# Optimization experiments

Hardware: AMD Instinct MI355X
Metric: run time of the kernel (lower is better)

The kernel has to match this reference:

```python
import jax, jax.numpy as jnp
import numpy as np

N_NODES = 50000


def _gcn_layer(x, W, b, src, dst, n_nodes):
    # GCNConv: h = D^{-1/2} (A + I) D^{-1/2} (x W) + b, with src/dst already
    # including self-loops.
    h = x @ W  # [N, out]
    deg = jax.ops.segment_sum(jnp.ones(src.shape, x.dtype), dst,
                              num_segments=n_nodes)  # [N]
    dinv = jnp.where(deg > 0, jax.lax.rsqrt(jnp.maximum(deg, 1e-12)), 0.0)
    norm = dinv[src] * dinv[dst]  # [E+N]
    msg = h[src] * norm[:, None]  # gathered + weighted messages
    out = jax.ops.segment_sum(msg, dst, num_segments=n_nodes)  # scatter-add
    return out + b


def setup_inputs() -> dict:
    key = jax.random.key(0)
    k0, k1, k2, k3 = jax.random.split(key, 4)
    d_in, hidden, n_edges = 128, 128, 800000
    x = jax.random.normal(k0, (N_NODES, d_in), dtype=jnp.float32)
    edge_index = jax.random.randint(k1, (2, n_edges), 0, N_NODES, dtype=jnp.int64)
    W1 = jax.random.normal(k2, (d_in, hidden), dtype=jnp.float32) * (1.0 / np.sqrt(d_in))
    b1 = jnp.zeros((hidden,), jnp.float32)
    W2 = jax.random.normal(k3, (hidden, hidden), dtype=jnp.float32) * (1.0 / np.sqrt(hidden))
    b2 = jnp.zeros((hidden,), jnp.float32)
    return {"x": x, "edge_index": edge_index, "W1": W1, "b1": b1,
            "W2": W2, "b2": b2}


def reference(x, edge_index, W1, b1, W2, b2):
    n = x.shape[0]
    loop = jnp.arange(n, dtype=edge_index.dtype)
    src = jnp.concatenate([edge_index[0], loop])  # add self-loops
    dst = jnp.concatenate([edge_index[1], loop])
    h = _gcn_layer(x, W1, b1, src, dst, n)
    h = jax.nn.relu(h)
    # dropout p=0.5 is identity in eval mode (self.training == False)
    h = _gcn_layer(h, W2, b2, src, dst, n)
    return jax.nn.log_softmax(h, axis=1)
```

## Files before the change

### kernel.cpp

```cpp
#include <hip/hip_runtime.h>
#include <math.h>

#define D 128
#define CAP 6144
#define EPB 4096

typedef __attribute__((ext_vector_type(8))) short bf16x8;
typedef __attribute__((ext_vector_type(4))) float f32x4;

__device__ __forceinline__ float bf_lo(unsigned u) { return __uint_as_float(u << 16); }
__device__ __forceinline__ float bf_hi(unsigned u) { return __uint_as_float(u & 0xFFFF0000u); }
__device__ __forceinline__ unsigned pack_bf16(float a, float b) {
    unsigned ua = __float_as_uint(a), ub = __float_as_uint(b);
    ua = (ua + 0x7FFFu + ((ua >> 16) & 1u)) >> 16;
    ub = (ub + 0x7FFFu + ((ub >> 16) & 1u)) >> 16;
    return ua | (ub << 16);
}

__device__ __forceinline__ int edge_at(const void* eidx, int i64, long long pos) {
    return i64 ? (int)((const long long*)eidx)[pos] : ((const int*)eidx)[pos];
}


__global__ void k_init(const int* e32, int* flag, int* bcnt) {
    int t = threadIdx.x;
    bcnt[t] = 0;
    if (t == 0) {
        int f = 1;
        #pragma unroll
        for (int j = 1; j < 32; j += 2)
            if (e32[j] != 0) f = 0;
        *flag = f;
    }
}


template <int AF32>
__device__ __forceinline__ void gemm_body(char* lds, int bid, const void* Ain,
                                          const float* __restrict__ Wf,
                                          unsigned* __restrict__ yout, int n) {
    int tid = threadIdx.x;
    #pragma unroll
    for (int it = 0; it < 32; ++it) {
        int idx = tid + it * 256;
        int c = idx & 127, k2 = idx >> 7;
        *(unsigned*)&lds[c * 272 + k2 * 4] =
            pack_bf16(Wf[(k2 * 2) * D + c], Wf[(k2 * 2 + 1) * D + c]);
    }
    int w = tid >> 6, l = tid & 63;
    int row0 = bid * 128;
    int rowA0 = row0 + w * 16 + (l & 15);
    int rowA1 = rowA0 + 64;
    int rA0 = rowA0 < n ? rowA0 : 0;
    int rA1 = rowA1 < n ? rowA1 : 0;
    __syncthreads();

    f32x4 acc[2][8];
    #pragma unroll
    for (int r = 0; r < 2; ++r)
        #pragma unroll
        for (int f = 0; f < 8; ++f) acc[r][f] = (f32x4)0.f;

    #pragma unroll
    for (int s = 0; s < 4; ++s) {
        bf16x8 a0, a1;
        if (AF32) {
            const float* Af = (const float*)Ain;
            const float4* p0 = (const float4*)(Af + (size_t)rA0 * D + ((l >> 4) << 3) + s * 32);
            const float4* p1 = (const float4*)(Af + (size_t)rA1 * D + ((l >> 4) << 3) + s * 32);
            float4 f0 = p0[0], f1 = p0[1], f2 = p1[0], f3 = p1[1];
            uint4 v0, v1;
            v0.x = pack_bf16(f0.x, f0.y); v0.y = pack_bf16(f0.z, f0.w);
            v0.z = pack_bf16(f1.x, f1.y); v0.w = pack_bf16(f1.z, f1.w);
            v1.x = pack_bf16(f2.x, f2.y); v1.y = pack_bf16(f2.z, f2.w);
            v1.z = pack_bf16(f3.x, f3.y); v1.w = pack_bf16(f3.z, f3.w);
            a0 = *(bf16x8*)&v0;
            a1 = *(bf16x8*)&v1;
        } else {
            const char* Ab = (const char*)Ain;
            a0 = *(const bf16x8*)(Ab + (size_t)rA0 * 256 + ((l >> 4) << 4) + s * 64);
            a1 = *(const bf16x8*)(Ab + (size_t)rA1 * 256 + ((l >> 4) << 4) + s * 64);
        }
        int boff = ((l >> 4) << 4) + s * 64;
        #pragma unroll
        for (int f = 0; f < 8; ++f) {
            bf16x8 b = *(const bf16x8*)&lds[(f * 16 + (l & 15)) * 272 + boff];
            acc[0][f] = __builtin_amdgcn_mfma_f32_16x16x32_bf16(a0, b, acc[0][f], 0, 0, 0);
            acc[1][f] = __builtin_amdgcn_mfma_f32_16x16x32_bf16(a1, b, acc[1][f], 0, 0, 0);
        }
    }

    float* fl = (float*)lds;
    #pragma unroll
    for (int r = 0; r < 2; ++r) {
        __syncthreads();
        {
            int rbase = w * 16 + ((l >> 4) << 2);
            #pragma unroll
            for (int f = 0; f < 8; ++f) {
                int c = f * 16 + (l & 15);
                #pragma unroll
                for (int j = 0; j < 4; ++j)
                    fl[(rbase + j) * 132 + c] = acc[r][f][j];
            }
        }
        __syncthreads();
        int row = tid >> 2, cseg = (tid & 3) << 5;
        int gr = row0 + r * 64 + row;
        if (gr < n) {
            uint4* ob = (uint4*)yout + (size_t)gr * 16 + ((tid & 3) << 2);
            #pragma unroll
            for (int q = 0; q < 4; ++q) {
                uint4 v;
                v.x = pack_bf16(fl[row * 132 + cseg + q * 8 + 0], fl[row * 132 + cseg + q * 8 + 1]);
                v.y = pack_bf16(fl[row * 132 + cseg + q * 8 + 2], fl[row * 132 + cseg + q * 8 + 3]);
                v.z = pack_bf16(fl[row * 132 + cseg + q * 8 + 4], fl[row * 132 + cseg + q * 8 + 5]);
                v.w = pack_bf16(fl[row * 132 + cseg + q * 8 + 6], fl[row * 132 + cseg + q * 8 + 7]);
                ob[q] = v;
            }
        }
    }
}


__global__ void __launch_bounds__(256) k_prep(const void* eidx, const int* flag,
                                              int* bcnt,
                                              unsigned* __restrict__ binned, int e,
                                              const float* __restrict__ x,
                                              const float* __restrict__ W1,
                                              unsigned* __restrict__ y1,
                                              int n, int ebk) {
    __shared__ char lds[35840];
    int b = blockIdx.x, t = threadIdx.x;

    if (b < ebk) {
        int* hist = (int*)lds;
        int* gbase = hist + 256;
        int* lcur = gbase + 256;
        uint2* ed = (uint2*)(lds + 3072);
        hist[t] = 0;
        lcur[t] = 0;
        __syncthreads();
        long long base = (long long)b * EPB;
        int i64 = *flag;
        #pragma unroll
        for (int k = 0; k < EPB / 256; ++k) {
            long long i = base + k * 256 + t;
            if (i < e) {
                int s = edge_at(eidx, i64, i);
                int d = edge_at(eidx, i64, (long long)e + i);
                ed[k * 256 + t] = make_uint2((unsigned)s, (unsigned)d);
                atomicAdd(&hist[d >> 8], 1);
            }
        }
        __syncthreads();
        int c = hist[t];
        gbase[t] = c ? atomicAdd(&bcnt[t], c) : 0;
        __syncthreads();
        long long rem = e - base;
        int lim = (rem < EPB) ? (int)rem : EPB;
        for (int j = t; j < lim; j += 256) {
            uint2 sd = ed[j];
            int bk = sd.y >> 8;
            int off = gbase[bk] + atomicAdd(&lcur[bk], 1);
            if (off >= CAP) off = CAP - 1;
            binned[(size_t)bk * CAP + off] = sd.x | ((sd.y & 255u) << 17);
        }
    } else {
        gemm_body<1>(lds, b - ebk, x, W1, y1, n);
    }
}


__global__ void __launch_bounds__(256) k_binB(const unsigned* __restrict__ binned,
                                              const int* __restrict__ bcnt,
                                              unsigned* __restrict__ meta,
                                              unsigned* __restrict__ csr64,
                                              int n) {
    __shared__ int lcur[256];
    int b = blockIdx.x, t = threadIdx.x;
    lcur[t] = 0;
    __syncthreads();

    int cnt = bcnt[b];
    if (cnt > CAP) cnt = CAP;
    unsigned nodebase = (unsigned)b << 8;
    for (int i = t; i < cnt; i += 256) {
        unsigned en = binned[(size_t)b * CAP + i];
        unsigned src = en & 0x1FFFF;
        unsigned dl = en >> 17;
        int pos = atomicAdd(&lcur[dl], 1);
        unsigned node = nodebase + dl;
        if (pos < 64)
            csr64[(size_t)node * 64 + pos] = src;
    }
    __syncthreads();

    int node = b * 256 + t;
    if (node < n) {
        int dv = lcur[t];
        unsigned q = __float2uint_rn(rsqrtf((float)(dv + 1)) * 32767.0f);
        meta[node] = (q << 17) | (unsigned)(dv < 64 ? dv : 64);
        int filled = dv < 64 ? dv : 64;
        int pend = (filled + 15) & ~15;
        for (int j = filled; j < pend; ++j)
            csr64[(size_t)node * 64 + j] = (unsigned)node;
    }
}


template <int EPI>
__global__ void __launch_bounds__(256) k_agg(const unsigned* __restrict__ Y,
                                             const unsigned* __restrict__ meta,
                                             const unsigned* __restrict__ csr64,
                                             const float* __restrict__ bias,
                                             void* __restrict__ outp, int n) {
    int node = blockIdx.x * 4 + (threadIdx.x >> 6);
    if (node >= n) return;
    int lane = threadIdx.x & 63;
    int l16 = lane & 15;
    unsigned mt = meta[node];
    unsigned us = Y[(size_t)node * 64 + lane];
    const unsigned* cp = csr64 + (size_t)node * 64;
    unsigned g0 = cp[l16];
    unsigned g1 = cp[16 + l16];

    int cdeg = mt & 0x1FFFF;
    float di = (float)(mt >> 17) * (1.0f / 32767.0f);
    int gcnt = (cdeg + 15) >> 4;
    float ax = 0.f, ay = 0.f;

#define PROCA(gv, base)                                                        \
    {                                                                          \
        unsigned uu[16], qq[16];                                               \
        _Pragma("unroll") for (int k2 = 0; k2 < 16; ++k2) {                    \
            unsigned s_ = __shfl((gv), k2, 16) & 0x1FFFF;                      \
            uu[k2] = Y[(size_t)s_ * 64 + lane];                                \
            qq[k2] = meta[s_];                                                 \
        }                                                                      \
        _Pragma("unroll") for (int k2 = 0; k2 < 16; ++k2) {                    \
            float w_ = ((base) + k2 < cdeg)                                    \
                           ? (float)(qq[k2] >> 17) * (1.0f / 32767.0f) : 0.f;  \
            ax += w_ * bf_lo(uu[k2]);                                          \
            ay += w_ * bf_hi(uu[k2]);                                          \
        }                                                                      \
    }

    if (gcnt > 0) PROCA(g0, 0);
    if (gcnt > 1) PROCA(g1, 16);
    if (gcnt > 2) {
        unsigned g2 = cp[32 + l16];
        if (gcnt > 3) {
            unsigned g3 = cp[48 + l16];
            PROCA(g2, 32);
            PROCA(g3, 48);
        } else {
            PROCA(g2, 32);
        }
    }
#undef PROCA

    float2 bv = ((const float2*)bias)[lane];
    float z0 = (ax + di * bf_lo(us)) * di + bv.x;
    float z1 = (ay + di * bf_hi(us)) * di + bv.y;

    if (EPI == 0) {
        ((unsigned*)outp)[(size_t)node * 64 + lane] =
            pack_bf16(fmaxf(z0, 0.f), fmaxf(z1, 0.f));
    } else {
        float m = fmaxf(z0, z1);
        #pragma unroll
        for (int off = 1; off < 64; off <<= 1) m = fmaxf(m, __shfl_xor(m, off));
        float s = __expf(z0 - m) + __expf(z1 - m);
        #pragma unroll
        for (int off = 1; off < 64; off <<= 1) s += __shfl_xor(s, off);
        float lse = m + __logf(s);
        ((float2*)outp)[(size_t)node * 64 + lane] = make_float2(z0 - lse, z1 - lse);
    }
}


__global__ void __launch_bounds__(256) k_gemm2(const unsigned* __restrict__ h,
                                               const float* __restrict__ W2,
                                               unsigned* __restrict__ y2, int n) {
    __shared__ char lds[34816];
    gemm_body<0>(lds, blockIdx.x, h, W2, y2, n);
}


extern "C" void kernel_launch(void* const* d_in, const int* in_sizes, int n_in,
                              void* d_out, int out_size, void* d_ws, size_t ws_size,
                              hipStream_t stream) {
    const float* x  = (const float*)d_in[0];
    const void* eix = d_in[1];
    const float* W1 = (const float*)d_in[2];
    const float* b1 = (const float*)d_in[3];
    const float* W2 = (const float*)d_in[4];
    const float* b2 = (const float*)d_in[5];
    float* out = (float*)d_out;
    int n = in_sizes[0] / D;
    int e = in_sizes[1] / 2;

    char* p = (char*)d_ws;
    auto carve = [&](size_t bytes) -> void* {
        void* r = (void*)p;
        p += (bytes + 255) & ~(size_t)255;
        return r;
    };
    int*      flag   = (int*)carve(4);
    unsigned* meta   = (unsigned*)carve((size_t)n * 4);
    int*      bcnt   = (int*)carve(1024);
    unsigned* csr64  = (unsigned*)carve((size_t)n * 64 * 4);
    unsigned* binned = (unsigned*)carve((size_t)256 * CAP * 4);
    unsigned* y1     = (unsigned*)carve((size_t)n * 64 * 4);
    unsigned* h      = (unsigned*)carve((size_t)n * 64 * 4);

    int nb = (n + 255) / 256;
    int ebk = (e + EPB - 1) / EPB;
    int gb = (n + 127) / 128;
    int ab = (n + 3) / 4;

    k_init<<<1, 256, 0, stream>>>((const int*)eix, flag, bcnt);
    k_prep<<<ebk + gb, 256, 0, stream>>>(eix, flag, bcnt, binned, e, x, W1, y1, n, ebk);
    k_binB<<<nb, 256, 0, stream>>>(binned, bcnt, meta, csr64, n);
    k_agg<0><<<ab, 256, 0, stream>>>(y1, meta, csr64, b1, h, n);
    k_gemm2<<<gb, 256, 0, stream>>>(h, W2, y1, n);
    k_agg<1><<<ab, 256, 0, stream>>>(y1, meta, csr64, b2, out, n);
}
```

Measured before the change: 135.3 us.

## Move layer-1 GEMM into CSR-build kernel and simplify aggregation to scalar-indexed loop

The layer-1 GEMM blocks now launch together with the CSR build (k_mid) instead of with the edge-binning pass. The edge-binning kernel becomes its own smaller launch. The aggregation kernel makes the node index wave-uniform and reads neighbor indices as scalars in 4-way unrolled loops. This replaces the 16-wide shuffle batches and drops the CSR padding writes. The per-edge scale factor is folded into a single final multiply. The intent is to balance the work that overlaps across the launch stages and to cut wasted padded gathers, at the cost of fewer gathers in flight per iteration.

```diff
diff --git a/kernel.cpp b/kernel.cpp
--- a/kernel.cpp
+++ b/kernel.cpp
@@ -31,6 +31,46 @@
         for (int j = 1; j < 32; j += 2)
             if (e32[j] != 0) f = 0;
         *flag = f;
+    }
+}
+
+
+__global__ void __launch_bounds__(256) k_prep(const void* eidx, const int* flag,
+                                              int* bcnt,
+                                              unsigned* __restrict__ binned, int e) {
+    __shared__ int hist[256];
+    __shared__ int gbase[256];
+    __shared__ int lcur[256];
+    __shared__ uint2 ed[EPB];
+    int b = blockIdx.x, t = threadIdx.x;
+
+    hist[t] = 0;
+    lcur[t] = 0;
+    __syncthreads();
+    long long base = (long long)b * EPB;
+    int i64 = *flag;
+    #pragma unroll
+    for (int k = 0; k < EPB / 256; ++k) {
+        long long i = base + k * 256 + t;
+        if (i < e) {
+            int s = edge_at(eidx, i64, i);
+            int d = edge_at(eidx, i64, (long long)e + i);
+            ed[k * 256 + t] = make_uint2((unsigned)s, (unsigned)d);
+            atomicAdd(&hist[d >> 8], 1);
+        }
+    }
+    __syncthreads();
+    int c = hist[t];
+    gbase[t] = c ? atomicAdd(&bcnt[t], c) : 0;
+    __syncthreads();
+    long long rem = e - base;
+    int lim = (rem < EPB) ? (int)rem : EPB;
+    for (int j = t; j < lim; j += 256) {
+        uint2 sd = ed[j];
+        int bk = sd.y >> 8;
+        int off = gbase[bk] + atomicAdd(&lcur[bk], 1);
+        if (off >= CAP) off = CAP - 1;
+        binned[(size_t)bk * CAP + off] = sd.x | ((sd.y & 255u) << 17);
     }
 }
 
@@ -123,62 +163,21 @@
 }
 
 
-__global__ void __launch_bounds__(256) k_prep(const void* eidx, const int* flag,
-                                              int* bcnt,
-                                              unsigned* __restrict__ binned, int e,
-                                              const float* __restrict__ x,
-                                              const float* __restrict__ W1,
-                                              unsigned* __restrict__ y1,
-                                              int n, int ebk) {
-    __shared__ char lds[35840];
+__global__ void __launch_bounds__(256) k_mid(const unsigned* __restrict__ binned,
+                                             const int* __restrict__ bcnt,
+                                             unsigned* __restrict__ meta,
+                                             unsigned* __restrict__ csr64,
+                                             const float* __restrict__ x,
+                                             const float* __restrict__ W1,
+                                             unsigned* __restrict__ y1,
+                                             int n, int nb) {
+    __shared__ char lds[34816];
     int b = blockIdx.x, t = threadIdx.x;
-
-    if (b < ebk) {
-        int* hist = (int*)lds;
-        int* gbase = hist + 256;
-        int* lcur = gbase + 256;
-        uint2* ed = (uint2*)(lds + 3072);
-        hist[t] = 0;
-        lcur[t] = 0;
-        __syncthreads();
-        long long base = (long long)b * EPB;
-        int i64 = *flag;
-        #pragma unroll
-        for (int k = 0; k < EPB / 256; ++k) {
-            long long i = base + k * 256 + t;
-            if (i < e) {
-                int s = edge_at(eidx, i64, i);
-                int d = edge_at(eidx, i64, (long long)e + i);
-                ed[k * 256 + t] = make_uint2((unsigned)s, (unsigned)d);
-                atomicAdd(&hist[d >> 8], 1);
-            }
-        }
-        __syncthreads();
-        int c = hist[t];
-        gbase[t] = c ? atomicAdd(&bcnt[t], c) : 0;
-        __syncthreads();
-        long long rem = e - base;
-        int lim = (rem < EPB) ? (int)rem : EPB;
-        for (int j = t; j < lim; j += 256) {
-            uint2 sd = ed[j];
-            int bk = sd.y >> 8;
-            int off = gbase[bk] + atomicAdd(&lcur[bk], 1);
-            if (off >= CAP) off = CAP - 1;
-            binned[(size_t)bk * CAP + off] = sd.x | ((sd.y & 255u) << 17);
-        }
-    } else {
-        gemm_body<1>(lds, b - ebk, x, W1, y1, n);
-    }
-}
-
-
-__global__ void __launch_bounds__(256) k_binB(const unsigned* __restrict__ binned,
-                                              const int* __restrict__ bcnt,
-                                              unsigned* __restrict__ meta,
-                                              unsigned* __restrict__ csr64,
-                                              int n) {
-    __shared__ int lcur[256];
-    int b = blockIdx.x, t = threadIdx.x;
+    if (b >= nb) {
+        gemm_body<1>(lds, b - nb, x, W1, y1, n);
+        return;
+    }
+    int* lcur = (int*)lds;
     lcur[t] = 0;
     __syncthreads();
 
@@ -201,10 +200,6 @@
         int dv = lcur[t];
         unsigned q = __float2uint_rn(rsqrtf((float)(dv + 1)) * 32767.0f);
         meta[node] = (q << 17) | (unsigned)(dv < 64 ? dv : 64);
-        int filled = dv < 64 ? dv : 64;
-        int pend = (filled + 15) & ~15;
-        for (int j = filled; j < pend; ++j)
-            csr64[(size_t)node * 64 + j] = (unsigned)node;
     }
 }
 
@@ -215,54 +210,44 @@
                                              const unsigned* __restrict__ csr64,
                                              const float* __restrict__ bias,
                                              void* __restrict__ outp, int n) {
-    int node = blockIdx.x * 4 + (threadIdx.x >> 6);
+    int node = __builtin_amdgcn_readfirstlane(blockIdx.x * 4 + (threadIdx.x >> 6));
     if (node >= n) return;
     int lane = threadIdx.x & 63;
-    int l16 = lane & 15;
     unsigned mt = meta[node];
     unsigned us = Y[(size_t)node * 64 + lane];
     const unsigned* cp = csr64 + (size_t)node * 64;
-    unsigned g0 = cp[l16];
-    unsigned g1 = cp[16 + l16];
 
     int cdeg = mt & 0x1FFFF;
     float di = (float)(mt >> 17) * (1.0f / 32767.0f);
-    int gcnt = (cdeg + 15) >> 4;
     float ax = 0.f, ay = 0.f;
 
-#define PROCA(gv, base)                                                        \
-    {                                                                          \
-        unsigned uu[16], qq[16];                                               \
-        _Pragma("unroll") for (int k2 = 0; k2 < 16; ++k2) {                    \
-            unsigned s_ = __shfl((gv), k2, 16) & 0x1FFFF;                      \
-            uu[k2] = Y[(size_t)s_ * 64 + lane];                                \
-            qq[k2] = meta[s_];                                                 \
-        }                                                                      \
-        _Pragma("unroll") for (int k2 = 0; k2 < 16; ++k2) {                    \
-            float w_ = ((base) + k2 < cdeg)                                    \
-                           ? (float)(qq[k2] >> 17) * (1.0f / 32767.0f) : 0.f;  \
-            ax += w_ * bf_lo(uu[k2]);                                          \
-            ay += w_ * bf_hi(uu[k2]);                                          \
-        }                                                                      \
-    }
-
-    if (gcnt > 0) PROCA(g0, 0);
-    if (gcnt > 1) PROCA(g1, 16);
-    if (gcnt > 2) {
-        unsigned g2 = cp[32 + l16];
-        if (gcnt > 3) {
-            unsigned g3 = cp[48 + l16];
-            PROCA(g2, 32);
-            PROCA(g3, 48);
-        } else {
-            PROCA(g2, 32);
-        }
-    }
-#undef PROCA
-
+    int k = 0;
+    for (; k + 4 <= cdeg; k += 4) {
+        unsigned s0 = cp[k + 0], s1 = cp[k + 1], s2 = cp[k + 2], s3 = cp[k + 3];
+        unsigned u0 = Y[(size_t)s0 * 64 + lane];
+        unsigned u1 = Y[(size_t)s1 * 64 + lane];
+        unsigned u2 = Y[(size_t)s2 * 64 + lane];
+        unsigned u3 = Y[(size_t)s3 * 64 + lane];
+        float q0 = (float)(meta[s0] >> 17);
+        float q1 = (float)(meta[s1] >> 17);
+        float q2 = (float)(meta[s2] >> 17);
+        float q3 = (float)(meta[s3] >> 17);
+        ax += q0 * bf_lo(u0) + q1 * bf_lo(u1) + q2 * bf_lo(u2) + q3 * bf_lo(u3);
+        ay += q0 * bf_hi(u0) + q1 * bf_hi(u1) + q2 * bf_hi(u2) + q3 * bf_hi(u3);
+    }
+    for (; k < cdeg; ++k) {
+        unsigned s0 = cp[k];
+        unsigned u0 = Y[(size_t)s0 * 64 + lane];
+        float q0 = (float)(meta[s0] >> 17);
+        ax += q0 * bf_lo(u0);
+        ay += q0 * bf_hi(u0);
+    }
+
+    float sc = di * (1.0f / 32767.0f);
+    float dd = di * di;
     float2 bv = ((const float2*)bias)[lane];
-    float z0 = (ax + di * bf_lo(us)) * di + bv.x;
-    float z1 = (ay + di * bf_hi(us)) * di + bv.y;
+    float z0 = ax * sc + dd * bf_lo(us) + bv.x;
+    float z1 = ay * sc + dd * bf_hi(us) + bv.y;
 
     if (EPI == 0) {
         ((unsigned*)outp)[(size_t)node * 64 + lane] =
@@ -321,8 +306,8 @@
     int ab = (n + 3) / 4;
 
     k_init<<<1, 256, 0, stream>>>((const int*)eix, flag, bcnt);
-    k_prep<<<ebk + gb, 256, 0, stream>>>(eix, flag, bcnt, binned, e, x, W1, y1, n, ebk);
-    k_binB<<<nb, 256, 0, stream>>>(binned, bcnt, meta, csr64, n);
+    k_prep<<<ebk, 256, 0, stream>>>(eix, flag, bcnt, binned, e);
+    k_mid<<<nb + gb, 256, 0, stream>>>(binned, bcnt, meta, csr64, x, W1, y1, n, nb);
     k_agg<0><<<ab, 256, 0, stream>>>(y1, meta, csr64, b1, h, n);
     k_gemm2<<<gb, 256, 0, stream>>>(h, W2, y1, n);
     k_agg<1><<<ab, 256, 0, stream>>>(y1, meta, csr64, b2, out, n);
```

Result: no change. 137.8 us (+1.9%).

## Pad CSR with zero dummy node, use scalar neighbor loads, drop init kernel

Applied to the files above, without the earlier changes.

Aggregation padding slots now point to an extra all-zero node (row n of y1, meta[n]=0), so the per-edge degree mask goes away. The neighbor loop reads CSR indices through a wave-uniform pointer (readfirstlane node), which allows scalar loads instead of per-lane loads plus shuffles. Meta stores the group count directly. The separate init kernel is replaced by a memset, with each prep block detecting the index dtype itself. Bins are padded with sentinel entries. The costs are an extra zero row, redundant flag checks in every block, and a runtime-bounded outer loop in place of the hand-unrolled group branches.

```diff
diff --git a/kernel.cpp b/kernel.cpp
--- a/kernel.cpp
+++ b/kernel.cpp
@@ -4,6 +4,7 @@
 #define D 128
 #define CAP 6144
 #define EPB 4096
+#define SENT 0xFFFFFFFFu
 
 typedef __attribute__((ext_vector_type(8))) short bf16x8;
 typedef __attribute__((ext_vector_type(4))) float f32x4;
@@ -19,19 +20,6 @@
 
 __device__ __forceinline__ int edge_at(const void* eidx, int i64, long long pos) {
     return i64 ? (int)((const long long*)eidx)[pos] : ((const int*)eidx)[pos];
-}
-
-
-__global__ void k_init(const int* e32, int* flag, int* bcnt) {
-    int t = threadIdx.x;
-    bcnt[t] = 0;
-    if (t == 0) {
-        int f = 1;
-        #pragma unroll
-        for (int j = 1; j < 32; j += 2)
-            if (e32[j] != 0) f = 0;
-        *flag = f;
-    }
 }
 
 
@@ -123,8 +111,7 @@
 }
 
 
-__global__ void __launch_bounds__(256) k_prep(const void* eidx, const int* flag,
-                                              int* bcnt,
+__global__ void __launch_bounds__(256) k_prep(const void* eidx, int* bcnt,
                                               unsigned* __restrict__ binned, int e,
                                               const float* __restrict__ x,
                                               const float* __restrict__ W1,
@@ -133,42 +120,54 @@
     __shared__ char lds[35840];
     int b = blockIdx.x, t = threadIdx.x;
 
-    if (b < ebk) {
-        int* hist = (int*)lds;
-        int* gbase = hist + 256;
-        int* lcur = gbase + 256;
-        uint2* ed = (uint2*)(lds + 3072);
-        hist[t] = 0;
-        lcur[t] = 0;
-        __syncthreads();
-        long long base = (long long)b * EPB;
-        int i64 = *flag;
-        #pragma unroll
-        for (int k = 0; k < EPB / 256; ++k) {
-            long long i = base + k * 256 + t;
-            if (i < e) {
-                int s = edge_at(eidx, i64, i);
-                int d = edge_at(eidx, i64, (long long)e + i);
-                ed[k * 256 + t] = make_uint2((unsigned)s, (unsigned)d);
-                atomicAdd(&hist[d >> 8], 1);
-            }
-        }
-        __syncthreads();
-        int c = hist[t];
-        gbase[t] = c ? atomicAdd(&bcnt[t], c) : 0;
-        __syncthreads();
-        long long rem = e - base;
-        int lim = (rem < EPB) ? (int)rem : EPB;
-        for (int j = t; j < lim; j += 256) {
-            uint2 sd = ed[j];
-            int bk = sd.y >> 8;
-            int off = gbase[bk] + atomicAdd(&lcur[bk], 1);
-            if (off >= CAP) off = CAP - 1;
-            binned[(size_t)bk * CAP + off] = sd.x | ((sd.y & 255u) << 17);
-        }
-    } else {
+    if (b >= ebk) {
         gemm_body<1>(lds, b - ebk, x, W1, y1, n);
-    }
+        return;
+    }
+
+    int* hist = (int*)lds;
+    int* gbase = hist + 256;
+    int* lcur = gbase + 256;
+    uint2* ed = (uint2*)(lds + 3072);
+
+    const int* e32 = (const int*)eidx;
+    int i64 = 1;
+    #pragma unroll
+    for (int j = 1; j < 32; j += 2)
+        if (e32[j] != 0) i64 = 0;
+
+    hist[t] = 0;
+    lcur[t] = 0;
+    __syncthreads();
+    long long base = (long long)b * EPB;
+    #pragma unroll
+    for (int k = 0; k < EPB / 256; ++k) {
+        long long i = base + k * 256 + t;
+        if (i < e) {
+            int s = edge_at(eidx, i64, i);
+            int d = edge_at(eidx, i64, (long long)e + i);
+            ed[k * 256 + t] = make_uint2((unsigned)s, (unsigned)d);
+            atomicAdd(&hist[d >> 8], 1);
+        }
+    }
+    __syncthreads();
+    int c = hist[t];
+    int cpad = (c + 15) & ~15;
+    gbase[t] = cpad ? atomicAdd(&bcnt[t], cpad) : 0;
+    __syncthreads();
+    long long rem = e - base;
+    int lim = (rem < EPB) ? (int)rem : EPB;
+    for (int j = t; j < lim; j += 256) {
+        uint2 sd = ed[j];
+        int bk = sd.y >> 8;
+        int off = gbase[bk] + atomicAdd(&lcur[bk], 1);
+        if (off >= CAP) off = CAP - 1;
+        binned[(size_t)bk * CAP + off] = sd.x | ((sd.y & 255u) << 17);
+    }
+    __syncthreads();
+    int gb_ = gbase[t];
+    for (int j = c; j < cpad; ++j)
+        binned[(size_t)t * CAP + gb_ + j] = SENT;
 }
 
 
@@ -176,9 +175,14 @@
                                               const int* __restrict__ bcnt,
                                               unsigned* __restrict__ meta,
                                               unsigned* __restrict__ csr64,
+                                              unsigned* __restrict__ y1,
                                               int n) {
     __shared__ int lcur[256];
     int b = blockIdx.x, t = threadIdx.x;
+    if (b == 0) {
+        if (t < 64) y1[(size_t)n * 64 + t] = 0;
+        if (t == 64) meta[n] = 0;
+    }
     lcur[t] = 0;
     __syncthreads();
 
@@ -187,24 +191,24 @@
     unsigned nodebase = (unsigned)b << 8;
     for (int i = t; i < cnt; i += 256) {
         unsigned en = binned[(size_t)b * CAP + i];
+        if (en == SENT) continue;
         unsigned src = en & 0x1FFFF;
         unsigned dl = en >> 17;
         int pos = atomicAdd(&lcur[dl], 1);
-        unsigned node = nodebase + dl;
         if (pos < 64)
-            csr64[(size_t)node * 64 + pos] = src;
+            csr64[(size_t)(nodebase + dl) * 64 + pos] = src;
     }
     __syncthreads();
 
     int node = b * 256 + t;
     if (node < n) {
         int dv = lcur[t];
-        unsigned q = __float2uint_rn(rsqrtf((float)(dv + 1)) * 32767.0f);
-        meta[node] = (q << 17) | (unsigned)(dv < 64 ? dv : 64);
         int filled = dv < 64 ? dv : 64;
         int pend = (filled + 15) & ~15;
         for (int j = filled; j < pend; ++j)
-            csr64[(size_t)node * 64 + j] = (unsigned)node;
+            csr64[(size_t)node * 64 + j] = (unsigned)n;
+        unsigned q = __float2uint_rn(rsqrtf((float)(dv + 1)) * 32767.0f);
+        meta[node] = (q << 17) | (unsigned)(pend >> 4);
     }
 }
 
@@ -215,54 +219,31 @@
                                              const unsigned* __restrict__ csr64,
                                              const float* __restrict__ bias,
                                              void* __restrict__ outp, int n) {
-    int node = blockIdx.x * 4 + (threadIdx.x >> 6);
+    int node = __builtin_amdgcn_readfirstlane(blockIdx.x * 4 + (threadIdx.x >> 6));
     if (node >= n) return;
     int lane = threadIdx.x & 63;
-    int l16 = lane & 15;
     unsigned mt = meta[node];
     unsigned us = Y[(size_t)node * 64 + lane];
     const unsigned* cp = csr64 + (size_t)node * 64;
-    unsigned g0 = cp[l16];
-    unsigned g1 = cp[16 + l16];
-
-    int cdeg = mt & 0x1FFFF;
+
+    int gcnt = mt & 7;
     float di = (float)(mt >> 17) * (1.0f / 32767.0f);
-    int gcnt = (cdeg + 15) >> 4;
     float ax = 0.f, ay = 0.f;
 
-#define PROCA(gv, base)                                                        \
-    {                                                                          \
-        unsigned uu[16], qq[16];                                               \
-        _Pragma("unroll") for (int k2 = 0; k2 < 16; ++k2) {                    \
-            unsigned s_ = __shfl((gv), k2, 16) & 0x1FFFF;                      \
-            uu[k2] = Y[(size_t)s_ * 64 + lane];                                \
-            qq[k2] = meta[s_];                                                 \
-        }                                                                      \
-        _Pragma("unroll") for (int k2 = 0; k2 < 16; ++k2) {                    \
-            float w_ = ((base) + k2 < cdeg)                                    \
-                           ? (float)(qq[k2] >> 17) * (1.0f / 32767.0f) : 0.f;  \
-            ax += w_ * bf_lo(uu[k2]);                                          \
-            ay += w_ * bf_hi(uu[k2]);                                          \
-        }                                                                      \
-    }
-
-    if (gcnt > 0) PROCA(g0, 0);
-    if (gcnt > 1) PROCA(g1, 16);
-    if (gcnt > 2) {
-        unsigned g2 = cp[32 + l16];
-        if (gcnt > 3) {
-            unsigned g3 = cp[48 + l16];
-            PROCA(g2, 32);
-            PROCA(g3, 48);
-        } else {
-            PROCA(g2, 32);
-        }
-    }
-#undef PROCA
+    for (int g = 0; g < gcnt; ++g) {
+        #pragma unroll
+        for (int k2 = 0; k2 < 16; ++k2) {
+            unsigned s_ = cp[g * 16 + k2];
+            float q = (float)(meta[s_] >> 17);
+            unsigned u = Y[(size_t)s_ * 64 + lane];
+            ax += q * bf_lo(u);
+            ay += q * bf_hi(u);
+        }
+    }
 
     float2 bv = ((const float2*)bias)[lane];
-    float z0 = (ax + di * bf_lo(us)) * di + bv.x;
-    float z1 = (ay + di * bf_hi(us)) * di + bv.y;
+    float z0 = di * (ax * (1.0f / 32767.0f) + di * bf_lo(us)) + bv.x;
+    float z1 = di * (ay * (1.0f / 32767.0f) + di * bf_hi(us)) + bv.y;
 
     if (EPI == 0) {
         ((unsigned*)outp)[(size_t)node * 64 + lane] =
@@ -307,12 +288,11 @@
         p += (bytes + 255) & ~(size_t)255;
         return r;
     };
-    int*      flag   = (int*)carve(4);
-    unsigned* meta   = (unsigned*)carve((size_t)n * 4);
+    unsigned* meta   = (unsigned*)carve((size_t)(n + 1) * 4);
     int*      bcnt   = (int*)carve(1024);
     unsigned* csr64  = (unsigned*)carve((size_t)n * 64 * 4);
     unsigned* binned = (unsigned*)carve((size_t)256 * CAP * 4);
-    unsigned* y1     = (unsigned*)carve((size_t)n * 64 * 4);
+    unsigned* y1     = (unsigned*)carve((size_t)(n + 1) * 64 * 4);
     unsigned* h      = (unsigned*)carve((size_t)n * 64 * 4);
 
     int nb = (n + 255) / 256;
@@ -320,9 +300,9 @@
     int gb = (n + 127) / 128;
     int ab = (n + 3) / 4;
 
-    k_init<<<1, 256, 0, stream>>>((const int*)eix, flag, bcnt);
-    k_prep<<<ebk + gb, 256, 0, stream>>>(eix, flag, bcnt, binned, e, x, W1, y1, n, ebk);
-    k_binB<<<nb, 256, 0, stream>>>(binned, bcnt, meta, csr64, n);
+    hipMemsetAsync(bcnt, 0, 1024, stream);
+    k_prep<<<ebk + gb, 256, 0, stream>>>(eix, bcnt, binned, e, x, W1, y1, n, ebk);
+    k_binB<<<nb, 256, 0, stream>>>(binned, bcnt, meta, csr64, y1, n);
     k_agg<0><<<ab, 256, 0, stream>>>(y1, meta, csr64, b1, h, n);
     k_gemm2<<<gb, 256, 0, stream>>>(h, W2, y1, n);
     k_agg<1><<<ab, 256, 0, stream>>>(y1, meta, csr64, b2, out, n);
```

Measured after the change: 145.1 us. +7.3%, slower.
